# Kernel optimization log

Measured on AMD Instinct MI355X. Metric: run time of the kernel, lower is better.

The kernel has to match this reference:

```python
import jax, jax.numpy as jnp
import numpy as np

N, CI, CO, K = 16384, 64, 64, 257


def setup_inputs() -> dict:
    key = jax.random.key(0)
    k1, k2 = jax.random.split(key)
    x = jax.random.normal(k1, (N, CI), dtype=jnp.float32)
    # lecun_normal-like scale over fan_in = K*CI
    kernel = jax.random.normal(k2, (K, CI, CO), dtype=jnp.float32) * (1.0 / np.sqrt(K * CI))
    bias = jnp.zeros((CO,), dtype=jnp.float32)
    return {"x": x, "kernel": kernel, "bias": bias}


def reference(x, kernel, bias):
    # Faithful translation of fconv1d.__call__ with strides=1, padding='valid'.
    Ci = x.shape[-1]
    Co = kernel.shape[-1]
    # h: (K, Ci*Co), flattened row-major so column j -> (ci=j//Co, co=j%Co)
    h = jnp.reshape(kernel, (kernel.shape[0], Ci * Co))
    # y: (N, Ci*Co), tiled so column j -> ci = j % Ci (exactly as jnp.tile does)
    y = jnp.tile(x, (1, Co))
    # Ci*Co independent 1D 'valid' convolutions (true convolution, kernel flipped)
    zflat = jax.vmap(lambda a, b: jnp.convolve(a, b, mode='valid'),
                     in_axes=-1, out_axes=-1)(y, h)  # (Nout, Ci*Co)
    # reduce over Ci exactly as the original reshape/sum does
    z = zflat.T.reshape((Co, Ci, -1)).sum(axis=1).T  # (Nout, Co)
    sps = 1  # strides = 1
    return z[::sps, :] + bias[None, :]
```

## Files before the change

### kernel.cpp

```cpp
#include <hip/hip_runtime.h>

#define NN   16384
#define CIN  64
#define COUT 64
#define KW   257
#define NOUT (NN - KW + 1)
#define BM   256
#define NKCH 8

typedef __attribute__((ext_vector_type(8))) short short8;
typedef __attribute__((ext_vector_type(8))) unsigned short ushortx8;
typedef __attribute__((ext_vector_type(4))) float floatx4;
typedef unsigned short ushort_t;

__device__ __forceinline__ ushort_t f2bf(float f) {
  union { float f; unsigned u; } c; c.f = f;
  unsigned u = c.u;
  return (ushort_t)((u + 0x7FFFu + ((u >> 16) & 1u)) >> 16);
}
__device__ __forceinline__ float bf2f(ushort_t h) {
  union { unsigned u; float f; } c; c.u = ((unsigned)h) << 16;
  return c.f;
}

__device__ __forceinline__ void cp16(const void* g, void* l) {
  auto gp = (const __attribute__((address_space(1))) unsigned int*)(unsigned long long)(uintptr_t)g;
  auto lp = (__attribute__((address_space(3))) unsigned int*)(unsigned int)(uintptr_t)l;
  __builtin_amdgcn_global_load_lds(gp, lp, 16, 0, 0);
}

__global__ void prep_convert(const float* __restrict__ x, const float* __restrict__ w,
                             ushort_t* __restrict__ xs, ushort_t* __restrict__ wsz) {
  const int c = blockIdx.x * blockDim.x + threadIdx.x;
  const float* src;
  ushort_t* dst;
  if (c < 131072) {
    const int row = c >> 3, ch = c & 7;
    src = x + (size_t)row * 64 + ((ch ^ (row & 7)) << 3);
    dst = xs + (size_t)row * 64 + (ch << 3);
  } else {
    const int c2 = c - 131072;
    const int t = c2 >> 9, r = (c2 >> 3) & 63, ch = c2 & 7;
    src = w + (size_t)(256 - t) * 4096 + r * 64 + ((ch ^ (r & 7)) << 3);
    dst = wsz + (size_t)t * 4096 + r * 64 + (ch << 3);
  }
  float4 v0 = *(const float4*)src;
  float4 v1 = *(const float4*)(src + 4);
  ushortx8 o;
  o[0] = f2bf(v0.x); o[1] = f2bf(v0.y); o[2] = f2bf(v0.z); o[3] = f2bf(v0.w);
  o[4] = f2bf(v1.x); o[5] = f2bf(v1.y); o[6] = f2bf(v1.z); o[7] = f2bf(v1.w);
  *(ushortx8*)dst = o;
}

__global__ __launch_bounds__(256, 2) void conv_gemm(
    const ushort_t* __restrict__ xs, const ushort_t* __restrict__ wsz,
    ushort_t* __restrict__ part) {
  __shared__ __align__(128) char smem[288 * 128 + 2 * 16384];
  char* Alds = smem;
  char* Wlds = smem + 288 * 128;

  const int tid  = threadIdx.x;
  const int lane = tid & 63;
  const int w    = tid >> 6;
  const int lr   = lane & 15;
  const int lh   = lane >> 4;

  const int mblk = blockIdx.x;
  const int g    = blockIdx.y;
  const int n0   = mblk * BM;
  const int t0   = (g * KW) / NKCH;
  const int t1   = ((g + 1) * KW) / NKCH;
  const int Tc   = t1 - t0;
  const int NCf  = Tc >> 1;
  const bool odd = Tc & 1;

  const ushort_t* agbase = xs + (size_t)(n0 + t0) * 64;
#pragma unroll
  for (int i = 0; i < 9; ++i)
    cp16(agbase + ((w * 9 + i) << 9) + lane * 8, Alds + ((w * 9 + i) << 10));

  const ushort_t* wgbase = wsz + (size_t)t0 * 4096;
#pragma unroll
  for (int s = 0; s < 2; ++s)
#pragma unroll
    for (int i = 0; i < 2; ++i)
      cp16(wgbase + (size_t)s * 4096 + ((w * 2 + i) << 9) + lane * 8,
           Wlds + s * 8192 + (w * 2 + i) * 1024);
  __syncthreads();

  floatx4 acc[4][4];
#pragma unroll
  for (int m = 0; m < 4; ++m)
#pragma unroll
    for (int nb = 0; nb < 4; ++nb)
      acc[m][nb] = (floatx4){0.f, 0.f, 0.f, 0.f};

  auto compute_t = [&](int ttL, const char* Wl) {
#pragma unroll
    for (int kk = 0; kk < 2; ++kk) {
      short8 a[4], b[4];
#pragma unroll
      for (int m = 0; m < 4; ++m) {
        const int row = ttL + w * 64 + m * 16 + lr;
        a[m] = *(const short8*)(Alds + row * 128 + (((lh + 4 * kk) ^ (row & 7)) << 4));
      }
#pragma unroll
      for (int nb = 0; nb < 4; ++nb) {
        const int rw = nb * 16 + lr;
        b[nb] = *(const short8*)(Wl + rw * 128 + (((lh + 4 * kk) ^ (rw & 7)) << 4));
      }
#pragma unroll
      for (int m = 0; m < 4; ++m)
#pragma unroll
        for (int nb = 0; nb < 4; ++nb)
          acc[m][nb] = __builtin_amdgcn_mfma_f32_16x16x32_bf16(a[m], b[nb], acc[m][nb], 0, 0, 0);
    }
  };

  for (int cc = 0; cc < NCf; ++cc) {
    const int buf = cc & 1;
    if (cc + 1 < NCf) {
      const ushort_t* wg = wsz + (size_t)(t0 + (cc + 1) * 2) * 4096;
#pragma unroll
      for (int s = 0; s < 2; ++s)
#pragma unroll
        for (int i = 0; i < 2; ++i)
          cp16(wg + (size_t)s * 4096 + ((w * 2 + i) << 9) + lane * 8,
               Wlds + (buf ^ 1) * 16384 + s * 8192 + (w * 2 + i) * 1024);
    } else if (odd) {
      const ushort_t* wg = wsz + (size_t)(t0 + NCf * 2) * 4096;
#pragma unroll
      for (int i = 0; i < 2; ++i)
        cp16(wg + ((w * 2 + i) << 9) + lane * 8,
             Wlds + (buf ^ 1) * 16384 + (w * 2 + i) * 1024);
    }
    compute_t(cc * 2, Wlds + buf * 16384);
    compute_t(cc * 2 + 1, Wlds + buf * 16384 + 8192);
    __syncthreads();
  }
  if (odd) compute_t(Tc - 1, Wlds + (NCf & 1) * 16384);

  ushort_t* pg = part + (size_t)g * (NOUT * 64);
#pragma unroll
  for (int m = 0; m < 4; ++m)
#pragma unroll
    for (int nb = 0; nb < 4; ++nb)
#pragma unroll
      for (int r = 0; r < 4; ++r) {
        const int row = n0 + w * 64 + m * 16 + lh * 4 + r;
        const int col = nb * 16 + lr;
        pg[(size_t)row * 64 + col] = f2bf(acc[m][nb][r]);
      }
}

__global__ void reduce_out(const ushort_t* __restrict__ part, const float* __restrict__ bias,
                           float* __restrict__ out) {
  const int i = blockIdx.x * blockDim.x + threadIdx.x;
  if (i >= NOUT * 8) return;
  const int colbase = (i & 7) * 8;
  float s[8];
#pragma unroll
  for (int j = 0; j < 8; ++j) s[j] = bias[colbase + j];
#pragma unroll
  for (int gg = 0; gg < NKCH; ++gg) {
    ushortx8 p = *(const ushortx8*)(part + (size_t)gg * (NOUT * 64) + (size_t)i * 8);
#pragma unroll
    for (int j = 0; j < 8; ++j) s[j] += bf2f(p[j]);
  }
  float4 o0 = {s[0], s[1], s[2], s[3]};
  float4 o1 = {s[4], s[5], s[6], s[7]};
  *(float4*)(out + (size_t)i * 8) = o0;
  *(float4*)(out + (size_t)i * 8 + 4) = o1;
}

__global__ void naive_conv(const float* __restrict__ x, const float* __restrict__ w,
                           const float* __restrict__ bias, float* __restrict__ out) {
  const int idx = blockIdx.x * blockDim.x + threadIdx.x;
  if (idx >= NOUT * COUT) return;
  const int n = idx / COUT, co = idx % COUT;
  float s = bias[co];
  for (int t = 0; t < KW; ++t) {
    const float* xr = x + (size_t)(n + t) * CIN;
    const float* wr = w + (size_t)(KW - 1 - t) * CIN * COUT + (size_t)co * CIN;
#pragma unroll 8
    for (int ci = 0; ci < CIN; ++ci) s += xr[ci] * wr[ci];
  }
  out[idx] = s;
}

extern "C" void kernel_launch(void* const* d_in, const int* in_sizes, int n_in,
                              void* d_out, int out_size, void* d_ws, size_t ws_size,
                              hipStream_t stream) {
  const float* x    = (const float*)d_in[0];
  const float* kern = (const float*)d_in[1];
  const float* bias = (const float*)d_in[2];
  float* out = (float*)d_out;

  const size_t xs_b   = (size_t)NN * CIN * 2;
  const size_t ws_b   = (size_t)KW * CIN * COUT * 2;
  const size_t part_b = (size_t)NKCH * NOUT * COUT * 2;
  const size_t need   = xs_b + ws_b + part_b;

  if (ws_size < need) {
    naive_conv<<<(NOUT * COUT + 255) / 256, 256, 0, stream>>>(x, kern, bias, out);
    return;
  }

  ushort_t* xs   = (ushort_t*)d_ws;
  ushort_t* wsz  = xs + (size_t)NN * CIN;
  ushort_t* part = wsz + (size_t)KW * CIN * COUT;

  prep_convert<<<1026, 256, 0, stream>>>(x, kern, xs, wsz);
  conv_gemm<<<dim3(NOUT / BM, NKCH), 256, 0, stream>>>(xs, wsz, part);
  reduce_out<<<(NOUT * 8 + 255) / 256, 256, 0, stream>>>(part, bias, out);
}
```

Before: 44.73 us.

## Split MFMA loop into barrier-separated phases with priority and fine-grained vmcnt waits

Replaces the per-chunk __syncthreads with explicit s_barrier plus partial vmcnt waits, so the just-issued prefetch of the next W chunk can stay in flight while the current buffer is consumed. Each k-step becomes a phase: LDS reads, then a barrier and lgkmcnt wait, then 16 MFMAs at raised wave priority, then another barrier. The intent is to make waves alternate between LDS loads and MFMA bursts and reduce pipeline stalls. The cost is many more barriers per tile. Correctness depends on the hand-counted vmcnt values matching the outstanding loads, including the initial A/W loads.

```diff
diff --git a/kernel.cpp b/kernel.cpp
--- a/kernel.cpp
+++ b/kernel.cpp
@@ -95,26 +95,29 @@
     for (int nb = 0; nb < 4; ++nb)
       acc[m][nb] = (floatx4){0.f, 0.f, 0.f, 0.f};
 
-  auto compute_t = [&](int ttL, const char* Wl) {
-#pragma unroll
-    for (int kk = 0; kk < 2; ++kk) {
-      short8 a[4], b[4];
-#pragma unroll
-      for (int m = 0; m < 4; ++m) {
-        const int row = ttL + w * 64 + m * 16 + lr;
-        a[m] = *(const short8*)(Alds + row * 128 + (((lh + 4 * kk) ^ (row & 7)) << 4));
-      }
-#pragma unroll
-      for (int nb = 0; nb < 4; ++nb) {
-        const int rw = nb * 16 + lr;
-        b[nb] = *(const short8*)(Wl + rw * 128 + (((lh + 4 * kk) ^ (rw & 7)) << 4));
-      }
-#pragma unroll
-      for (int m = 0; m < 4; ++m)
-#pragma unroll
-        for (int nb = 0; nb < 4; ++nb)
-          acc[m][nb] = __builtin_amdgcn_mfma_f32_16x16x32_bf16(a[m], b[nb], acc[m][nb], 0, 0, 0);
+  auto phase = [&](int ttL, int kk, const char* Wl) {
+    short8 a[4], b[4];
+#pragma unroll
+    for (int m = 0; m < 4; ++m) {
+      const int row = ttL + w * 64 + m * 16 + lr;
+      a[m] = *(const short8*)(Alds + row * 128 + (((lh + 4 * kk) ^ (row & 7)) << 4));
     }
+#pragma unroll
+    for (int nb = 0; nb < 4; ++nb) {
+      const int rw = nb * 16 + lr;
+      b[nb] = *(const short8*)(Wl + rw * 128 + (((lh + 4 * kk) ^ (rw & 7)) << 4));
+    }
+    __builtin_amdgcn_s_barrier();
+    asm volatile("s_waitcnt lgkmcnt(0)" ::: "memory");
+    __builtin_amdgcn_sched_barrier(0);
+    __builtin_amdgcn_s_setprio(1);
+#pragma unroll
+    for (int m = 0; m < 4; ++m)
+#pragma unroll
+      for (int nb = 0; nb < 4; ++nb)
+        acc[m][nb] = __builtin_amdgcn_mfma_f32_16x16x32_bf16(a[m], b[nb], acc[m][nb], 0, 0, 0);
+    __builtin_amdgcn_s_setprio(0);
+    __builtin_amdgcn_s_barrier();
   };
 
   for (int cc = 0; cc < NCf; ++cc) {
@@ -127,18 +130,32 @@
         for (int i = 0; i < 2; ++i)
           cp16(wg + (size_t)s * 4096 + ((w * 2 + i) << 9) + lane * 8,
                Wlds + (buf ^ 1) * 16384 + s * 8192 + (w * 2 + i) * 1024);
+      asm volatile("s_waitcnt vmcnt(4)" ::: "memory");
     } else if (odd) {
       const ushort_t* wg = wsz + (size_t)(t0 + NCf * 2) * 4096;
 #pragma unroll
       for (int i = 0; i < 2; ++i)
         cp16(wg + ((w * 2 + i) << 9) + lane * 8,
              Wlds + (buf ^ 1) * 16384 + (w * 2 + i) * 1024);
+      asm volatile("s_waitcnt vmcnt(2)" ::: "memory");
+    } else {
+      asm volatile("s_waitcnt vmcnt(0)" ::: "memory");
     }
-    compute_t(cc * 2, Wlds + buf * 16384);
-    compute_t(cc * 2 + 1, Wlds + buf * 16384 + 8192);
-    __syncthreads();
-  }
-  if (odd) compute_t(Tc - 1, Wlds + (NCf & 1) * 16384);
+    __builtin_amdgcn_s_barrier();
+
+    const char* Wl = Wlds + buf * 16384;
+    phase(cc * 2,     0, Wl);
+    phase(cc * 2,     1, Wl);
+    phase(cc * 2 + 1, 0, Wl + 8192);
+    phase(cc * 2 + 1, 1, Wl + 8192);
+  }
+  if (odd) {
+    asm volatile("s_waitcnt vmcnt(0)" ::: "memory");
+    __builtin_amdgcn_s_barrier();
+    const char* Wl = Wlds + (NCf & 1) * 16384;
+    phase(Tc - 1, 0, Wl);
+    phase(Tc - 1, 1, Wl);
+  }
 
   ushort_t* pg = part + (size_t)g * (NOUT * 64);
 #pragma unroll
```

After: 45.45 us. No clear change (+1.6%).

## Switch to 32x32x16 MFMA with split-K across waves and LDS reduction

Applied to the files above, without the earlier changes.

Replaces the 16x16x32 bf16 MFMA tiling with 32x32x16 MFMAs. The four waves are split into two row halves times two K halves, and the K-split partials are reduced through shared memory. The epilogue now writes the partial tile with vectorized 16-byte stores instead of scattered 2-byte stores. Fewer LDS fragment loads are needed per MFMA, at the cost of an extra shared-memory reduction pass with added barriers.

```diff
diff --git a/kernel.cpp b/kernel.cpp
--- a/kernel.cpp
+++ b/kernel.cpp
@@ -10,7 +10,7 @@
 
 typedef __attribute__((ext_vector_type(8))) short short8;
 typedef __attribute__((ext_vector_type(8))) unsigned short ushortx8;
-typedef __attribute__((ext_vector_type(4))) float floatx4;
+typedef __attribute__((ext_vector_type(16))) float floatx16;
 typedef unsigned short ushort_t;
 
 __device__ __forceinline__ ushort_t f2bf(float f) {
@@ -62,8 +62,10 @@
   const int tid  = threadIdx.x;
   const int lane = tid & 63;
   const int w    = tid >> 6;
-  const int lr   = lane & 15;
-  const int lh   = lane >> 4;
+  const int l31  = lane & 31;
+  const int lh2  = lane >> 5;
+  const int rh   = w & 1;
+  const int ks   = w >> 1;
 
   const int mblk = blockIdx.x;
   const int g    = blockIdx.y;
@@ -88,32 +90,33 @@
            Wlds + s * 8192 + (w * 2 + i) * 1024);
   __syncthreads();
 
-  floatx4 acc[4][4];
+  floatx16 acc[4][2];
 #pragma unroll
   for (int m = 0; m < 4; ++m)
 #pragma unroll
-    for (int nb = 0; nb < 4; ++nb)
-      acc[m][nb] = (floatx4){0.f, 0.f, 0.f, 0.f};
-
-  auto compute_t = [&](int ttL, const char* Wl) {
-#pragma unroll
-    for (int kk = 0; kk < 2; ++kk) {
-      short8 a[4], b[4];
+    for (int n = 0; n < 2; ++n)
+      acc[m][n] = (floatx16)(0.f);
+
+  auto compute_tap = [&](int tt, const char* Wl) {
+#pragma unroll
+    for (int kk2 = 0; kk2 < 2; ++kk2) {
+      const int c0 = lh2 + 2 * (2 * ks + kk2);
+      short8 a[4], b[2];
 #pragma unroll
       for (int m = 0; m < 4; ++m) {
-        const int row = ttL + w * 64 + m * 16 + lr;
-        a[m] = *(const short8*)(Alds + row * 128 + (((lh + 4 * kk) ^ (row & 7)) << 4));
+        const int row = tt + rh * 128 + m * 32 + l31;
+        a[m] = *(const short8*)(Alds + row * 128 + ((c0 ^ (row & 7)) << 4));
       }
 #pragma unroll
-      for (int nb = 0; nb < 4; ++nb) {
-        const int rw = nb * 16 + lr;
-        b[nb] = *(const short8*)(Wl + rw * 128 + (((lh + 4 * kk) ^ (rw & 7)) << 4));
+      for (int n = 0; n < 2; ++n) {
+        const int rw = n * 32 + l31;
+        b[n] = *(const short8*)(Wl + rw * 128 + ((c0 ^ (rw & 7)) << 4));
       }
 #pragma unroll
       for (int m = 0; m < 4; ++m)
 #pragma unroll
-        for (int nb = 0; nb < 4; ++nb)
-          acc[m][nb] = __builtin_amdgcn_mfma_f32_16x16x32_bf16(a[m], b[nb], acc[m][nb], 0, 0, 0);
+        for (int n = 0; n < 2; ++n)
+          acc[m][n] = __builtin_amdgcn_mfma_f32_32x32x16_bf16(a[m], b[n], acc[m][n], 0, 0, 0);
     }
   };
 
@@ -134,23 +137,50 @@
         cp16(wg + ((w * 2 + i) << 9) + lane * 8,
              Wlds + (buf ^ 1) * 16384 + (w * 2 + i) * 1024);
     }
-    compute_t(cc * 2, Wlds + buf * 16384);
-    compute_t(cc * 2 + 1, Wlds + buf * 16384 + 8192);
+    compute_tap(cc * 2,     Wlds + buf * 16384);
+    compute_tap(cc * 2 + 1, Wlds + buf * 16384 + 8192);
     __syncthreads();
   }
-  if (odd) compute_t(Tc - 1, Wlds + (NCf & 1) * 16384);
-
-  ushort_t* pg = part + (size_t)g * (NOUT * 64);
-#pragma unroll
-  for (int m = 0; m < 4; ++m)
-#pragma unroll
-    for (int nb = 0; nb < 4; ++nb)
-#pragma unroll
-      for (int r = 0; r < 4; ++r) {
-        const int row = n0 + w * 64 + m * 16 + lh * 4 + r;
-        const int col = nb * 16 + lr;
-        pg[(size_t)row * 64 + col] = f2bf(acc[m][nb][r]);
-      }
+  if (odd) compute_tap(Tc - 1, Wlds + (NCf & 1) * 16384);
+
+  __syncthreads();
+  float* red = (float*)smem;
+  if (ks == 1) {
+#pragma unroll
+    for (int m = 0; m < 4; ++m)
+#pragma unroll
+      for (int n = 0; n < 2; ++n)
+#pragma unroll
+        for (int r = 0; r < 16; ++r) {
+          const int row = rh * 128 + m * 32 + (r & 3) + 8 * (r >> 2) + 4 * lh2;
+          red[row * 64 + n * 32 + l31] = acc[m][n][r];
+        }
+  }
+  __syncthreads();
+  if (ks == 0) {
+#pragma unroll
+    for (int m = 0; m < 4; ++m)
+#pragma unroll
+      for (int n = 0; n < 2; ++n)
+#pragma unroll
+        for (int r = 0; r < 16; ++r) {
+          const int row = rh * 128 + m * 32 + (r & 3) + 8 * (r >> 2) + 4 * lh2;
+          const int idx = row * 64 + n * 32 + l31;
+          red[idx] += acc[m][n][r];
+        }
+  }
+  __syncthreads();
+  ushort_t* pg = part + (size_t)g * (NOUT * 64) + (size_t)n0 * 64;
+#pragma unroll
+  for (int s = 0; s < 8; ++s) {
+    const int e = (tid + s * 256) * 8;
+    float4 f0 = *(const float4*)(red + e);
+    float4 f1 = *(const float4*)(red + e + 4);
+    ushortx8 o;
+    o[0] = f2bf(f0.x); o[1] = f2bf(f0.y); o[2] = f2bf(f0.z); o[3] = f2bf(f0.w);
+    o[4] = f2bf(f1.x); o[5] = f2bf(f1.y); o[6] = f2bf(f1.z); o[7] = f2bf(f1.w);
+    *(ushortx8*)(pg + e) = o;
+  }
 }
 
 __global__ void reduce_out(const ushort_t* __restrict__ part, const float* __restrict__ bias,
```

Result: slower. 47.86 us (+7.0%).
